# Performance work log

Hardware: AMD Instinct MI355X
Metric: run time of the kernel (lower is better)

The kernel has to match this reference:

```python
import jax, jax.numpy as jnp
import numpy as np

NUM_BASES = 8


def setup_inputs() -> dict:
    key = jax.random.key(0)
    ks = jax.random.split(key, 8)
    N, E = 100000, 1600000
    IN_F, OUT_F, NUM_RELS = 128, 128, 16
    si = IN_F // NUM_BASES   # 16
    so = OUT_F // NUM_BASES  # 16
    return {
        "h": jax.random.normal(ks[0], (N, IN_F), dtype=jnp.float32),
        "norm": jax.random.uniform(ks[1], (N, 1), dtype=jnp.float32),
        "edge_src": jax.random.randint(ks[2], (E,), 0, N, dtype=jnp.int32),
        "edge_dst": jax.random.randint(ks[3], (E,), 0, N, dtype=jnp.int32),
        "edge_type": jax.random.randint(ks[4], (E,), 0, NUM_RELS, dtype=jnp.int32),
        "weight": jax.random.normal(ks[5], (NUM_RELS, NUM_BASES * si * so), dtype=jnp.float32) * 0.1,
        "bias_param": jax.random.normal(ks[6], (OUT_F,), dtype=jnp.float32) * 0.1,
        "loop_weight": jax.random.normal(ks[7], (IN_F, OUT_F), dtype=jnp.float32) * 0.1,
    }


def reference(h, norm, edge_src, edge_dst, edge_type, weight, bias_param, loop_weight):
    N, in_feat = h.shape
    out_feat = loop_weight.shape[1]
    si = in_feat // NUM_BASES
    so = out_feat // NUM_BASES
    E = edge_type.shape[0]

    # self-loop message (dropout=0.0 -> identity)
    loop_message = h @ loop_weight                      # [N, out_feat]

    # msg_func: gather per-edge relation weight blocks and do block-diag bmm
    W = weight[edge_type].reshape(E, NUM_BASES, si, so)  # [E, B, si, so]
    src = h[edge_src].reshape(E, NUM_BASES, si)          # [E, B, si]
    msg = jnp.einsum("ebi,ebio->ebo", src, W).reshape(E, out_feat)

    # scatter-sum messages to destination nodes, rescale by norm
    agg = jax.ops.segment_sum(msg, edge_dst, num_segments=N)  # [N, out_feat]
    node_repr = agg * norm

    # bias + self-loop + activation
    node_repr = node_repr + bias_param + loop_message
    return jax.nn.relu(node_repr)
```

## Files before the change

### kernel.cpp

```cpp
#include <hip/hip_runtime.h>


typedef float nfloat4 __attribute__((ext_vector_type(4)));

__device__ __forceinline__ unsigned int f2bf(float f) {
  const unsigned int u = __float_as_uint(f);
  return (u + 0x7FFFu + ((u >> 16) & 1u)) >> 16;
}

__global__ __launch_bounds__(256) void rgcn_init_kernel(
    const float* __restrict__ h, const float* __restrict__ loop_w,
    const float* __restrict__ bias, float* __restrict__ out, int N) {
  __shared__ float lw[128 * 128];
  for (int idx = threadIdx.x; idx < 128 * 128 / 4; idx += 256) {
    ((float4*)lw)[idx] = ((const float4*)loop_w)[idx];
  }
  __syncthreads();

  const int lane = threadIdx.x & 63;
  const int wid = threadIdx.x >> 6;
  const int group0 = blockIdx.x * 4 + wid;
  const int ngroups = gridDim.x * 4;
  const int totgroups = (N + 3) >> 2;
  const float b0 = bias[lane];
  const float b1 = bias[64 + lane];

  for (int g = group0; g < totgroups; g += ngroups) {
    const int n0 = g * 4;
    const int nn = (N - n0 < 4) ? (N - n0) : 4;
    if (nn == 4) {
      const float* __restrict__ r0 = h + (size_t)n0 * 128;
      const float* __restrict__ r1 = r0 + 128;
      const float* __restrict__ r2 = r1 + 128;
      const float* __restrict__ r3 = r2 + 128;
      float a00 = b0, a01 = b1, a10 = b0, a11 = b1;
      float a20 = b0, a21 = b1, a30 = b0, a31 = b1;
#pragma unroll 4
      for (int k = 0; k < 128; ++k) {
        const float w0 = lw[k * 128 + lane];
        const float w1 = lw[k * 128 + 64 + lane];
        a00 = fmaf(r0[k], w0, a00); a01 = fmaf(r0[k], w1, a01);
        a10 = fmaf(r1[k], w0, a10); a11 = fmaf(r1[k], w1, a11);
        a20 = fmaf(r2[k], w0, a20); a21 = fmaf(r2[k], w1, a21);
        a30 = fmaf(r3[k], w0, a30); a31 = fmaf(r3[k], w1, a31);
      }
      float* __restrict__ o0 = out + (size_t)n0 * 128;
      o0[lane] = a00;        o0[64 + lane] = a01;
      o0[128 + lane] = a10;  o0[192 + lane] = a11;
      o0[256 + lane] = a20;  o0[320 + lane] = a21;
      o0[384 + lane] = a30;  o0[448 + lane] = a31;
    } else {
      for (int r = 0; r < nn; ++r) {
        const int n = n0 + r;
        const float* __restrict__ hr = h + (size_t)n * 128;
        float a0 = b0, a1 = b1;
#pragma unroll 4
        for (int k = 0; k < 128; ++k) {
          const float a = hr[k];
          a0 = fmaf(a, lw[k * 128 + lane], a0);
          a1 = fmaf(a, lw[k * 128 + 64 + lane], a1);
        }
        out[(size_t)n * 128 + lane] = a0;
        out[(size_t)n * 128 + 64 + lane] = a1;
      }
    }
  }
}

__global__ __launch_bounds__(1024) void rgcn_precompute_kernel(
    const float* __restrict__ h, const float* __restrict__ weight,
    unsigned int* __restrict__ M, int base, int cend) {
  __shared__ unsigned int st[4 * 1024];
  const int tid = threadIdx.x;
  const int lane = tid & 63;
  const int t = tid >> 6;
  const int b = lane >> 4;
  const int o = lane & 15;

  const float* __restrict__ wb = weight + t * 2048 + b * 256 + o;
  float wlo[16], whi[16];
#pragma unroll
  for (int i = 0; i < 16; ++i) {
    wlo[i] = wb[i * 16];
    whi[i] = wb[1024 + i * 16];
  }

  const int span = cend - base;
  const int ngroups = (span + 3) >> 2;

  for (int g = blockIdx.x; g < ngroups; g += gridDim.x) {
    const int n0 = base + g * 4;
#pragma unroll
    for (int j = 0; j < 4; ++j) {
      const int n = n0 + j;
      unsigned int pk = 0;
      if (n < cend) {
        const float4* __restrict__ hp =
            (const float4*)(h + (size_t)n * 128) + (b << 2);
        const float4 x0 = hp[0], x1 = hp[1], x2 = hp[2], x3 = hp[3];
        const float4 y0 = hp[16], y1 = hp[17], y2 = hp[18], y3 = hp[19];

        float a0 = x0.x * wlo[0], a1 = x0.y * wlo[1];
        a0 = fmaf(x0.z, wlo[2], a0);  a1 = fmaf(x0.w, wlo[3], a1);
        a0 = fmaf(x1.x, wlo[4], a0);  a1 = fmaf(x1.y, wlo[5], a1);
        a0 = fmaf(x1.z, wlo[6], a0);  a1 = fmaf(x1.w, wlo[7], a1);
        a0 = fmaf(x2.x, wlo[8], a0);  a1 = fmaf(x2.y, wlo[9], a1);
        a0 = fmaf(x2.z, wlo[10], a0); a1 = fmaf(x2.w, wlo[11], a1);
        a0 = fmaf(x3.x, wlo[12], a0); a1 = fmaf(x3.y, wlo[13], a1);
        a0 = fmaf(x3.z, wlo[14], a0); a1 = fmaf(x3.w, wlo[15], a1);

        float c0 = y0.x * whi[0], c1 = y0.y * whi[1];
        c0 = fmaf(y0.z, whi[2], c0);  c1 = fmaf(y0.w, whi[3], c1);
        c0 = fmaf(y1.x, whi[4], c0);  c1 = fmaf(y1.y, whi[5], c1);
        c0 = fmaf(y1.z, whi[6], c0);  c1 = fmaf(y1.w, whi[7], c1);
        c0 = fmaf(y2.x, whi[8], c0);  c1 = fmaf(y2.y, whi[9], c1);
        c0 = fmaf(y2.z, whi[10], c0); c1 = fmaf(y2.w, whi[11], c1);
        c0 = fmaf(y3.x, whi[12], c0); c1 = fmaf(y3.y, whi[13], c1);
        c0 = fmaf(y3.z, whi[14], c0); c1 = fmaf(y3.w, whi[15], c1);

        pk = f2bf(a0 + a1) | (f2bf(c0 + c1) << 16);
      }
      st[j * 1024 + tid] = pk;
    }
    __syncthreads();

    const size_t dst = ((size_t)(n0 - base)) << 10;
    if (n0 + 4 <= cend) {
      const nfloat4 v = ((const nfloat4*)st)[tid];
      __builtin_nontemporal_store(v, ((nfloat4*)(M + dst)) + tid);
    } else {
      const int valid = (cend - n0) << 10;
      for (int k = tid; k < valid; k += 1024) M[dst + k] = st[k];
    }
    __syncthreads();
  }
}

__global__ __launch_bounds__(256) void rgcn_zero_kernel(int* __restrict__ p,
                                                        int n) {
  for (int i = blockIdx.x * 256 + threadIdx.x; i < n; i += gridDim.x * 256)
    p[i] = 0;
}

__global__ __launch_bounds__(256) void rgcn_hist_kernel(
    const int* __restrict__ esrc, const int* __restrict__ edst,
    int* __restrict__ cnt, int E, int N, unsigned S) {
  for (int e = blockIdx.x * 256 + threadIdx.x; e < E; e += gridDim.x * 256) {
    const unsigned q = (unsigned)esrc[e] / S;
    atomicAdd(&cnt[(int)(q * (unsigned)N) + edst[e]], 1);
  }
}

__global__ __launch_bounds__(1024) void rgcn_scan_pass1(
    const int* __restrict__ cnt, int* __restrict__ partial, int bins) {
  __shared__ int sums[1024];
  const int t = threadIdx.x;
  const int base = blockIdx.x * 4096 + t * 4;
  int s = 0;
  if (base + 3 < bins) {
    const int4 v = *(const int4*)(cnt + base);
    s = v.x + v.y + v.z + v.w;
  } else {
    for (int j = 0; j < 4; ++j)
      if (base + j < bins) s += cnt[base + j];
  }
  sums[t] = s;
  __syncthreads();
  for (int off = 512; off > 0; off >>= 1) {
    if (t < off) sums[t] += sums[t + off];
    __syncthreads();
  }
  if (t == 0) partial[blockIdx.x] = sums[0];
}

__global__ __launch_bounds__(1024) void rgcn_scan_pass2(
    int* __restrict__ partial, int nb) {
  __shared__ int sc[1024];
  const int t = threadIdx.x;
  int v[4];
  int s = 0;
#pragma unroll
  for (int j = 0; j < 4; ++j) {
    const int i = t * 4 + j;
    v[j] = (i < nb) ? partial[i] : 0;
    s += v[j];
  }
  sc[t] = s;
  __syncthreads();
#pragma unroll
  for (int off = 1; off < 1024; off <<= 1) {
    const int add = (t >= off) ? sc[t - off] : 0;
    __syncthreads();
    sc[t] += add;
    __syncthreads();
  }
  int run = (t == 0) ? 0 : sc[t - 1];
#pragma unroll
  for (int j = 0; j < 4; ++j) {
    const int i = t * 4 + j;
    if (i < nb) partial[i] = run;
    run += v[j];
  }
}

__global__ __launch_bounds__(1024) void rgcn_scan_pass3(
    const int* __restrict__ cnt, const int* __restrict__ partial,
    int* __restrict__ row_ptr, int* __restrict__ cursor, int bins) {
  __shared__ int sums[1024];
  const int t = threadIdx.x;
  const int base = blockIdx.x * 4096 + t * 4;
  int v0 = 0, v1 = 0, v2 = 0, v3 = 0;
  if (base + 3 < bins) {
    const int4 v = *(const int4*)(cnt + base);
    v0 = v.x; v1 = v.y; v2 = v.z; v3 = v.w;
  } else {
    if (base < bins) v0 = cnt[base];
    if (base + 1 < bins) v1 = cnt[base + 1];
    if (base + 2 < bins) v2 = cnt[base + 2];
  }
  sums[t] = v0 + v1 + v2 + v3;
  __syncthreads();
#pragma unroll
  for (int off = 1; off < 1024; off <<= 1) {
    const int add = (t >= off) ? sums[t - off] : 0;
    __syncthreads();
    sums[t] += add;
    __syncthreads();
  }
  const int run = partial[blockIdx.x] + ((t == 0) ? 0 : sums[t - 1]);
  const int p0 = run, p1 = p0 + v0, p2 = p1 + v1, p3 = p2 + v2;
  if (base + 3 < bins) {
    *(int4*)(row_ptr + base) = make_int4(p0, p1, p2, p3);
    *(int4*)(cursor + base) = make_int4(p0, p1, p2, p3);
  } else {
    if (base < bins) { row_ptr[base] = p0; cursor[base] = p0; }
    if (base + 1 < bins) { row_ptr[base + 1] = p1; cursor[base + 1] = p1; }
    if (base + 2 < bins) { row_ptr[base + 2] = p2; cursor[base + 2] = p2; }
  }
}

__global__ void rgcn_set_kernel(int* __restrict__ p, int v) {
  if (threadIdx.x == 0) *p = v;
}

__global__ __launch_bounds__(256) void rgcn_scatter_kernel(
    const int* __restrict__ esrc, const int* __restrict__ edst,
    const int* __restrict__ etype, int* __restrict__ cursor,
    int* __restrict__ srec, int E, int N, unsigned S) {
  for (int e = blockIdx.x * 256 + threadIdx.x; e < E; e += gridDim.x * 256) {
    const unsigned s = (unsigned)esrc[e];
    const unsigned q = s / S;
    const int key = (int)(q * (unsigned)N) + edst[e];
    const int p = atomicAdd(&cursor[key], 1);
    srec[p] = (int)((s - q * S) << 4) | etype[e];
  }
}

__global__ __launch_bounds__(256) void rgcn_gather3_kernel(
    const float* __restrict__ norm, const int* __restrict__ srec,
    const int* __restrict__ rpc, const unsigned int* __restrict__ M,
    float* __restrict__ out, int N, int final_pass) {
  const int lane = threadIdx.x & 63;
  const int w0 = blockIdx.x * 4 + (threadIdx.x >> 6);
  const int nw = gridDim.x * 4;

  for (int d = w0; d < N; d += nw) {
    const int e0 = rpc[d];
    const int e1 = rpc[d + 1];
    if (!final_pass && e0 == e1) continue;

    float acc0 = 0.f, acc1 = 0.f;
    int e = e0;
    for (; e + 8 <= e1; e += 8) {
      const int r0 = srec[e], r1 = srec[e + 1], r2 = srec[e + 2],
                r3 = srec[e + 3], r4 = srec[e + 4], r5 = srec[e + 5],
                r6 = srec[e + 6], r7 = srec[e + 7];
      const unsigned int v0 = __builtin_nontemporal_load(&M[(size_t)r0 * 64 + lane]);
      const unsigned int v1 = __builtin_nontemporal_load(&M[(size_t)r1 * 64 + lane]);
      const unsigned int v2 = __builtin_nontemporal_load(&M[(size_t)r2 * 64 + lane]);
      const unsigned int v3 = __builtin_nontemporal_load(&M[(size_t)r3 * 64 + lane]);
      const unsigned int v4 = __builtin_nontemporal_load(&M[(size_t)r4 * 64 + lane]);
      const unsigned int v5 = __builtin_nontemporal_load(&M[(size_t)r5 * 64 + lane]);
      const unsigned int v6 = __builtin_nontemporal_load(&M[(size_t)r6 * 64 + lane]);
      const unsigned int v7 = __builtin_nontemporal_load(&M[(size_t)r7 * 64 + lane]);
      acc0 += __uint_as_float(v0 << 16);
      acc1 += __uint_as_float(v0 & 0xFFFF0000u);
      acc0 += __uint_as_float(v1 << 16);
      acc1 += __uint_as_float(v1 & 0xFFFF0000u);
      acc0 += __uint_as_float(v2 << 16);
      acc1 += __uint_as_float(v2 & 0xFFFF0000u);
      acc0 += __uint_as_float(v3 << 16);
      acc1 += __uint_as_float(v3 & 0xFFFF0000u);
      acc0 += __uint_as_float(v4 << 16);
      acc1 += __uint_as_float(v4 & 0xFFFF0000u);
      acc0 += __uint_as_float(v5 << 16);
      acc1 += __uint_as_float(v5 & 0xFFFF0000u);
      acc0 += __uint_as_float(v6 << 16);
      acc1 += __uint_as_float(v6 & 0xFFFF0000u);
      acc0 += __uint_as_float(v7 << 16);
      acc1 += __uint_as_float(v7 & 0xFFFF0000u);
    }
    for (; e + 4 <= e1; e += 4) {
      const int r0 = srec[e], r1 = srec[e + 1], r2 = srec[e + 2],
                r3 = srec[e + 3];
      const unsigned int v0 = __builtin_nontemporal_load(&M[(size_t)r0 * 64 + lane]);
      const unsigned int v1 = __builtin_nontemporal_load(&M[(size_t)r1 * 64 + lane]);
      const unsigned int v2 = __builtin_nontemporal_load(&M[(size_t)r2 * 64 + lane]);
      const unsigned int v3 = __builtin_nontemporal_load(&M[(size_t)r3 * 64 + lane]);
      acc0 += __uint_as_float(v0 << 16);
      acc1 += __uint_as_float(v0 & 0xFFFF0000u);
      acc0 += __uint_as_float(v1 << 16);
      acc1 += __uint_as_float(v1 & 0xFFFF0000u);
      acc0 += __uint_as_float(v2 << 16);
      acc1 += __uint_as_float(v2 & 0xFFFF0000u);
      acc0 += __uint_as_float(v3 << 16);
      acc1 += __uint_as_float(v3 & 0xFFFF0000u);
    }
    for (; e < e1; ++e) {
      const unsigned int v = __builtin_nontemporal_load(&M[(size_t)srec[e] * 64 + lane]);
      acc0 += __uint_as_float(v << 16);
      acc1 += __uint_as_float(v & 0xFFFF0000u);
    }

    const float nm = norm[d];
    float* __restrict__ op = out + ((size_t)d << 7);
    float o0 = fmaf(acc0, nm, op[lane]);
    float o1 = fmaf(acc1, nm, op[64 + lane]);
    if (final_pass) {
      o0 = fmaxf(o0, 0.f);
      o1 = fmaxf(o1, 0.f);
    }
    op[lane] = o0;
    op[64 + lane] = o1;
  }
}

__global__ __launch_bounds__(256) void rgcn_edge_kernel(
    const float* __restrict__ h, const float* __restrict__ norm,
    const int* __restrict__ esrc, const int* __restrict__ edst,
    const int* __restrict__ etype, const float* __restrict__ weight,
    float* __restrict__ out, int E) {
  const int lane = threadIdx.x & 63;
  const int wid = threadIdx.x >> 6;
  const int wave0 = blockIdx.x * 4 + wid;
  const int nwaves = gridDim.x * 4;
  const int b = lane >> 4;
  const int o = lane & 15;

  for (int e = wave0; e < E; e += nwaves) {
    const int src = esrc[e];
    const int dst = edst[e];
    const int et = etype[e];
    const float s_lo = h[src * 128 + lane];
    const float s_hi = h[src * 128 + 64 + lane];
    const float nrm = norm[dst];
    const float* __restrict__ Wb = weight + et * 2048 + b * 256 + o;
    float m0 = 0.f, m1 = 0.f;
#pragma unroll
    for (int i = 0; i < 16; ++i) {
      const float a_lo = __shfl(s_lo, (lane & 48) + i, 64);
      const float a_hi = __shfl(s_hi, (lane & 48) + i, 64);
      m0 = fmaf(a_lo, Wb[i * 16], m0);
      m1 = fmaf(a_hi, Wb[1024 + i * 16], m1);
    }
    atomicAdd(&out[dst * 128 + lane], m0 * nrm);
    atomicAdd(&out[dst * 128 + 64 + lane], m1 * nrm);
  }
}

__global__ __launch_bounds__(256) void rgcn_relu_kernel(float* __restrict__ out,
                                                        int total4) {
  int i = blockIdx.x * 256 + threadIdx.x;
  const int stride = gridDim.x * 256;
  for (; i < total4; i += stride) {
    float4 v = ((float4*)out)[i];
    v.x = fmaxf(v.x, 0.f);
    v.y = fmaxf(v.y, 0.f);
    v.z = fmaxf(v.z, 0.f);
    v.w = fmaxf(v.w, 0.f);
    ((float4*)out)[i] = v;
  }
}

extern "C" void kernel_launch(void* const* d_in, const int* in_sizes, int n_in,
                              void* d_out, int out_size, void* d_ws, size_t ws_size,
                              hipStream_t stream) {
  const float* h      = (const float*)d_in[0];
  const float* norm   = (const float*)d_in[1];
  const int*   esrc   = (const int*)d_in[2];
  const int*   edst   = (const int*)d_in[3];
  const int*   etype  = (const int*)d_in[4];
  const float* weight = (const float*)d_in[5];
  const float* bias   = (const float*)d_in[6];
  const float* loop_w = (const float*)d_in[7];
  float* out = (float*)d_out;

  const int N = in_sizes[0] / 128;
  const int E = in_sizes[2];
  const int nrels = in_sizes[5] / 2048;

  rgcn_init_kernel<<<2048, 256, 0, stream>>>(h, loop_w, bias, out, N);

  int C = -1, S = 0;
  size_t ofs_rp = 0, ofs_cur = 0, ofs_part = 0, ofs_srec = 0, ofs_M = 0;
  if (nrels == 16 && N >= 1 && N < (1 << 26)) {
    for (int cc = 1; cc <= 64; ++cc) {
      const size_t bins = (size_t)cc * (size_t)N;
      if (bins > (size_t)4096 * 4096) break;
      const int ss = (N + cc - 1) / cc;
      const size_t o_rp = (bins + 3) & ~(size_t)3;
      const size_t o_cur = (o_rp + bins + 1 + 3) & ~(size_t)3;
      const size_t o_part = (o_cur + bins + 3) & ~(size_t)3;
      const size_t o_srec = o_part + 4096;
      const size_t o_M = (o_srec + (size_t)E + 15) & ~(size_t)15;
      const size_t need = (o_M + (size_t)ss * 16 * 64) * 4;
      if (need <= ws_size) {
        C = cc; S = ss;
        ofs_rp = o_rp; ofs_cur = o_cur; ofs_part = o_part;
        ofs_srec = o_srec; ofs_M = o_M;
        break;
      }
    }
  }

  if (C >= 1) {
    const int bins = C * N;
    const int nb = (bins + 4095) / 4096;
    int* base    = (int*)d_ws;
    int* cnt     = base;
    int* row_ptr = base + ofs_rp;
    int* cursor  = base + ofs_cur;
    int* partial = base + ofs_part;
    int* srec    = base + ofs_srec;
    unsigned int* M = (unsigned int*)(base + ofs_M);

    rgcn_zero_kernel<<<1024, 256, 0, stream>>>(cnt, bins);
    rgcn_hist_kernel<<<2048, 256, 0, stream>>>(esrc, edst, cnt, E, N,
                                               (unsigned)S);
    rgcn_scan_pass1<<<nb, 1024, 0, stream>>>(cnt, partial, bins);
    rgcn_scan_pass2<<<1, 1024, 0, stream>>>(partial, nb);
    rgcn_scan_pass3<<<nb, 1024, 0, stream>>>(cnt, partial, row_ptr, cursor,
                                             bins);
    rgcn_set_kernel<<<1, 64, 0, stream>>>(row_ptr + bins, E);
    rgcn_scatter_kernel<<<2048, 256, 0, stream>>>(esrc, edst, etype, cursor,
                                                  srec, E, N, (unsigned)S);
    for (int c = 0; c < C; ++c) {
      const int cbase = c * S;
      const int cend = (cbase + S < N) ? (cbase + S) : N;
      if (cbase >= N) break;
      rgcn_precompute_kernel<<<512, 1024, 0, stream>>>(h, weight, M, cbase,
                                                       cend);
      rgcn_gather3_kernel<<<2048, 256, 0, stream>>>(
          norm, srec, row_ptr + (size_t)c * N, M, out, N,
          (c == C - 1) ? 1 : 0);
    }
  } else {
    rgcn_edge_kernel<<<4096, 256, 0, stream>>>(h, norm, esrc, edst, etype,
                                               weight, out, E);
    rgcn_relu_kernel<<<2048, 256, 0, stream>>>(out, (N * 128) / 4);
  }
}
```

Measured before the change: 887.1 us.

## Store self-loop message as bf16 in workspace and fuse it into the final gather

The self-loop matmul plus bias now writes a packed bf16 buffer in the workspace instead of fp32 into the output. The gather passes accumulate raw sums in the output: the first pass writes without reading, and the final pass applies norm, adds the bf16 loop term and applies ReLU. This halves the traffic for the loop-message write, removes the initial read of the output, and drops the 4-wide tail loop. In exchange it rounds the loop message to bf16, and the workspace must now hold an extra N*64 words.

```diff
diff --git a/kernel.cpp b/kernel.cpp
--- a/kernel.cpp
+++ b/kernel.cpp
@@ -8,9 +8,9 @@
   return (u + 0x7FFFu + ((u >> 16) & 1u)) >> 16;
 }
 
-__global__ __launch_bounds__(256) void rgcn_init_kernel(
+__global__ __launch_bounds__(256) void rgcn_loopm_kernel(
     const float* __restrict__ h, const float* __restrict__ loop_w,
-    const float* __restrict__ bias, float* __restrict__ out, int N) {
+    const float* __restrict__ bias, unsigned int* __restrict__ loopm, int N) {
   __shared__ float lw[128 * 128];
   for (int idx = threadIdx.x; idx < 128 * 128 / 4; idx += 256) {
     ((float4*)lw)[idx] = ((const float4*)loop_w)[idx];
@@ -44,11 +44,10 @@
         a20 = fmaf(r2[k], w0, a20); a21 = fmaf(r2[k], w1, a21);
         a30 = fmaf(r3[k], w0, a30); a31 = fmaf(r3[k], w1, a31);
       }
-      float* __restrict__ o0 = out + (size_t)n0 * 128;
-      o0[lane] = a00;        o0[64 + lane] = a01;
-      o0[128 + lane] = a10;  o0[192 + lane] = a11;
-      o0[256 + lane] = a20;  o0[320 + lane] = a21;
-      o0[384 + lane] = a30;  o0[448 + lane] = a31;
+      loopm[(size_t)(n0 + 0) * 64 + lane] = f2bf(a00) | (f2bf(a01) << 16);
+      loopm[(size_t)(n0 + 1) * 64 + lane] = f2bf(a10) | (f2bf(a11) << 16);
+      loopm[(size_t)(n0 + 2) * 64 + lane] = f2bf(a20) | (f2bf(a21) << 16);
+      loopm[(size_t)(n0 + 3) * 64 + lane] = f2bf(a30) | (f2bf(a31) << 16);
     } else {
       for (int r = 0; r < nn; ++r) {
         const int n = n0 + r;
@@ -60,9 +59,41 @@
           a0 = fmaf(a, lw[k * 128 + lane], a0);
           a1 = fmaf(a, lw[k * 128 + 64 + lane], a1);
         }
-        out[(size_t)n * 128 + lane] = a0;
-        out[(size_t)n * 128 + 64 + lane] = a1;
+        loopm[(size_t)n * 64 + lane] = f2bf(a0) | (f2bf(a1) << 16);
       }
+    }
+  }
+}
+
+__global__ __launch_bounds__(256) void rgcn_init_kernel(
+    const float* __restrict__ h, const float* __restrict__ loop_w,
+    const float* __restrict__ bias, float* __restrict__ out, int N) {
+  __shared__ float lw[128 * 128];
+  for (int idx = threadIdx.x; idx < 128 * 128 / 4; idx += 256) {
+    ((float4*)lw)[idx] = ((const float4*)loop_w)[idx];
+  }
+  __syncthreads();
+  const int lane = threadIdx.x & 63;
+  const int wid = threadIdx.x >> 6;
+  const int group0 = blockIdx.x * 4 + wid;
+  const int ngroups = gridDim.x * 4;
+  const float b0 = bias[lane];
+  const float b1 = bias[64 + lane];
+  for (int g = group0; g < (N + 3) >> 2; g += ngroups) {
+    const int n0 = g * 4;
+    const int nn = (N - n0 < 4) ? (N - n0) : 4;
+    for (int r = 0; r < nn; ++r) {
+      const int n = n0 + r;
+      const float* __restrict__ hr = h + (size_t)n * 128;
+      float a0 = b0, a1 = b1;
+#pragma unroll 4
+      for (int k = 0; k < 128; ++k) {
+        const float a = hr[k];
+        a0 = fmaf(a, lw[k * 128 + lane], a0);
+        a1 = fmaf(a, lw[k * 128 + 64 + lane], a1);
+      }
+      out[(size_t)n * 128 + lane] = a0;
+      out[(size_t)n * 128 + 64 + lane] = a1;
     }
   }
 }
@@ -259,15 +290,18 @@
 __global__ __launch_bounds__(256) void rgcn_gather3_kernel(
     const float* __restrict__ norm, const int* __restrict__ srec,
     const int* __restrict__ rpc, const unsigned int* __restrict__ M,
-    float* __restrict__ out, int N, int final_pass) {
+    const unsigned int* __restrict__ loopm, float* __restrict__ out, int N,
+    int mode) {
   const int lane = threadIdx.x & 63;
   const int w0 = blockIdx.x * 4 + (threadIdx.x >> 6);
   const int nw = gridDim.x * 4;
+  const bool first = (mode & 1) != 0;
+  const bool final_pass = (mode & 2) != 0;
 
   for (int d = w0; d < N; d += nw) {
     const int e0 = rpc[d];
     const int e1 = rpc[d + 1];
-    if (!final_pass && e0 == e1) continue;
+    if (!first && !final_pass && e0 == e1) continue;
 
     float acc0 = 0.f, acc1 = 0.f;
     int e = e0;
@@ -300,38 +334,27 @@
       acc0 += __uint_as_float(v7 << 16);
       acc1 += __uint_as_float(v7 & 0xFFFF0000u);
     }
-    for (; e + 4 <= e1; e += 4) {
-      const int r0 = srec[e], r1 = srec[e + 1], r2 = srec[e + 2],
-                r3 = srec[e + 3];
-      const unsigned int v0 = __builtin_nontemporal_load(&M[(size_t)r0 * 64 + lane]);
-      const unsigned int v1 = __builtin_nontemporal_load(&M[(size_t)r1 * 64 + lane]);
-      const unsigned int v2 = __builtin_nontemporal_load(&M[(size_t)r2 * 64 + lane]);
-      const unsigned int v3 = __builtin_nontemporal_load(&M[(size_t)r3 * 64 + lane]);
-      acc0 += __uint_as_float(v0 << 16);
-      acc1 += __uint_as_float(v0 & 0xFFFF0000u);
-      acc0 += __uint_as_float(v1 << 16);
-      acc1 += __uint_as_float(v1 & 0xFFFF0000u);
-      acc0 += __uint_as_float(v2 << 16);
-      acc1 += __uint_as_float(v2 & 0xFFFF0000u);
-      acc0 += __uint_as_float(v3 << 16);
-      acc1 += __uint_as_float(v3 & 0xFFFF0000u);
-    }
     for (; e < e1; ++e) {
       const unsigned int v = __builtin_nontemporal_load(&M[(size_t)srec[e] * 64 + lane]);
       acc0 += __uint_as_float(v << 16);
       acc1 += __uint_as_float(v & 0xFFFF0000u);
     }
 
-    const float nm = norm[d];
     float* __restrict__ op = out + ((size_t)d << 7);
-    float o0 = fmaf(acc0, nm, op[lane]);
-    float o1 = fmaf(acc1, nm, op[64 + lane]);
+    if (!first) {
+      acc0 += op[lane];
+      acc1 += op[64 + lane];
+    }
     if (final_pass) {
-      o0 = fmaxf(o0, 0.f);
-      o1 = fmaxf(o1, 0.f);
-    }
-    op[lane] = o0;
-    op[64 + lane] = o1;
+      const float nm = norm[d];
+      const unsigned int lp = loopm[(size_t)d * 64 + lane];
+      op[lane] = fmaxf(fmaf(acc0, nm, __uint_as_float(lp << 16)), 0.f);
+      op[64 + lane] =
+          fmaxf(fmaf(acc1, nm, __uint_as_float(lp & 0xFFFF0000u)), 0.f);
+    } else {
+      op[lane] = acc0;
+      op[64 + lane] = acc1;
+    }
   }
 }
 
@@ -399,10 +422,9 @@
   const int E = in_sizes[2];
   const int nrels = in_sizes[5] / 2048;
 
-  rgcn_init_kernel<<<2048, 256, 0, stream>>>(h, loop_w, bias, out, N);
-
   int C = -1, S = 0;
-  size_t ofs_rp = 0, ofs_cur = 0, ofs_part = 0, ofs_srec = 0, ofs_M = 0;
+  size_t ofs_rp = 0, ofs_cur = 0, ofs_part = 0, ofs_srec = 0, ofs_lpm = 0,
+         ofs_M = 0;
   if (nrels == 16 && N >= 1 && N < (1 << 26)) {
     for (int cc = 1; cc <= 64; ++cc) {
       const size_t bins = (size_t)cc * (size_t)N;
@@ -412,12 +434,13 @@
       const size_t o_cur = (o_rp + bins + 1 + 3) & ~(size_t)3;
       const size_t o_part = (o_cur + bins + 3) & ~(size_t)3;
       const size_t o_srec = o_part + 4096;
-      const size_t o_M = (o_srec + (size_t)E + 15) & ~(size_t)15;
+      const size_t o_lpm = (o_srec + (size_t)E + 15) & ~(size_t)15;
+      const size_t o_M = o_lpm + (size_t)N * 64;
       const size_t need = (o_M + (size_t)ss * 16 * 64) * 4;
       if (need <= ws_size) {
         C = cc; S = ss;
         ofs_rp = o_rp; ofs_cur = o_cur; ofs_part = o_part;
-        ofs_srec = o_srec; ofs_M = o_M;
+        ofs_srec = o_srec; ofs_lpm = o_lpm; ofs_M = o_M;
         break;
       }
     }
@@ -432,8 +455,10 @@
     int* cursor  = base + ofs_cur;
     int* partial = base + ofs_part;
     int* srec    = base + ofs_srec;
-    unsigned int* M = (unsigned int*)(base + ofs_M);
-
+    unsigned int* loopm = (unsigned int*)(base + ofs_lpm);
+    unsigned int* M     = (unsigned int*)(base + ofs_M);
+
+    rgcn_loopm_kernel<<<2048, 256, 0, stream>>>(h, loop_w, bias, loopm, N);
     rgcn_zero_kernel<<<1024, 256, 0, stream>>>(cnt, bins);
     rgcn_hist_kernel<<<2048, 256, 0, stream>>>(esrc, edst, cnt, E, N,
                                                (unsigned)S);
@@ -450,11 +475,12 @@
       if (cbase >= N) break;
       rgcn_precompute_kernel<<<512, 1024, 0, stream>>>(h, weight, M, cbase,
                                                        cend);
+      const int mode = (c == 0 ? 1 : 0) | (c == C - 1 ? 2 : 0);
       rgcn_gather3_kernel<<<2048, 256, 0, stream>>>(
-          norm, srec, row_ptr + (size_t)c * N, M, out, N,
-          (c == C - 1) ? 1 : 0);
+          norm, srec, row_ptr + (size_t)c * N, M, loopm, out, N, mode);
     }
   } else {
+    rgcn_init_kernel<<<2048, 256, 0, stream>>>(h, loop_w, bias, out, N);
     rgcn_edge_kernel<<<4096, 256, 0, stream>>>(h, norm, esrc, edst, etype,
                                                weight, out, E);
     rgcn_relu_kernel<<<2048, 256, 0, stream>>>(out, (N * 128) / 4);
```

New measurement: 912.9 us. +2.9%, slower.
